# Optimization experiments

Hardware: AMD Instinct MI355X
Metric: run time of the kernel (lower is better)

Reference implementation:

```python
import jax, jax.numpy as jnp
import numpy as np

N_NODES = 100000
N_EDGES = 1600000
D = 128
HID = 256  # min(2*D, 256)
D_OUT = 128
BN_EPS = 1e-5


def setup_inputs() -> dict:
    key = jax.random.key(0)
    ks = jax.random.split(key, 16)
    s = 0.05
    inp = {
        "x": jax.random.normal(ks[0], (N_NODES, D), dtype=jnp.float32),
        "edges": jax.random.randint(ks[1], (2, N_EDGES), 0, N_NODES, dtype=jnp.int32),
        # affine_before_rnn: Linear(D, D)
        "W_aff": jax.random.normal(ks[2], (D, D), dtype=jnp.float32) * s,
        "b_aff": jnp.zeros((D,), dtype=jnp.float32),
        # GRUCell(D, D)
        "W_ih": jax.random.normal(ks[3], (3 * D, D), dtype=jnp.float32) * s,
        "b_ih": jnp.zeros((3 * D,), dtype=jnp.float32),
        "W_hh": jax.random.normal(ks[4], (3 * D, D), dtype=jnp.float32) * s,
        "b_hh": jnp.zeros((3 * D,), dtype=jnp.float32),
        # merge_layer: Linear(2*D, D)
        "W_merge": jax.random.normal(ks[5], (D, 2 * D), dtype=jnp.float32) * s,
        "b_merge": jnp.zeros((D,), dtype=jnp.float32),
        # learnable self-connection weight
        "eps": jnp.asarray(1.0, dtype=jnp.float32),
        # backbone: Linear(D, HID) -> relu -> Linear(HID, D_OUT) -> relu -> BatchNorm1d
        "W1": jax.random.normal(ks[6], (HID, D), dtype=jnp.float32) * s,
        "b1": jnp.zeros((HID,), dtype=jnp.float32),
        "W2": jax.random.normal(ks[7], (D_OUT, HID), dtype=jnp.float32) * s,
        "b2": jnp.zeros((D_OUT,), dtype=jnp.float32),
        "gamma": jnp.ones((D_OUT,), dtype=jnp.float32),
        "beta": jnp.zeros((D_OUT,), dtype=jnp.float32),
    }
    return inp


def reference(x, edges, W_aff, b_aff, W_ih, b_ih, W_hh, b_hh,
              W_merge, b_merge, eps, W1, b1, W2, b2, gamma, beta):
    src, dst = edges[0], edges[1]
    n = x.shape[0]

    # ---- aggregation 1: 'sum' -> scatter-sum of neighbor features ----
    agg_sum = jax.ops.segment_sum(x[src], dst, num_segments=n)  # (N, D)

    # ---- aggregation 2: 'rnn-max' -> affine, scatter-max, GRUCell ----
    xi = x @ W_aff.T + b_aff
    agg_max = jax.ops.segment_max(xi[src], dst, num_segments=n)  # (N, D)
    agg_max = jnp.where(jnp.isfinite(agg_max), agg_max, 0.0)  # empty segments -> 0

    # GRUCell: input = aggregated neighbors, hidden = original node features
    gi = agg_max @ W_ih.T + b_ih  # (N, 3D)
    gh = x @ W_hh.T + b_hh        # (N, 3D)
    ir, iz, inn = jnp.split(gi, 3, axis=1)
    hr, hz, hn = jnp.split(gh, 3, axis=1)
    r = jax.nn.sigmoid(ir + hr)
    z = jax.nn.sigmoid(iz + hz)
    ncand = jnp.tanh(inn + r * hn)
    rnn_out = (1.0 - z) * ncand + z * x  # (N, D)

    # ---- merge ('cat') ----
    h = jnp.concatenate([agg_sum, rnn_out], axis=1) @ W_merge.T + b_merge  # (N, D)

    # ---- learnable self-connection ----
    h = h + eps * x

    # ---- backbone: dense -> relu -> dense -> relu -> batchnorm1d (train mode) ----
    h = jax.nn.relu(h @ W1.T + b1)
    h = jax.nn.relu(h @ W2.T + b2)
    mean = jnp.mean(h, axis=0)
    var = jnp.mean(jnp.square(h - mean), axis=0)  # biased batch variance
    out = gamma * (h - mean) * jax.lax.rsqrt(var + BN_EPS) + beta
    return out
```

## Files before the change

### kernel.cpp

```cpp
#include <hip/hip_runtime.h>
#include <hip/hip_bf16.h>
#include <math.h>

using bf16 = __hip_bfloat16;
typedef __attribute__((ext_vector_type(8))) short bf16x8;
typedef __attribute__((ext_vector_type(4))) float f32x4;

__device__ __forceinline__ float b2f(unsigned short u) {
  return __uint_as_float(((unsigned)u) << 16);
}
__device__ __forceinline__ unsigned short f2b(float f) {
  bf16 h = __float2bfloat16(f);
  return *reinterpret_cast<unsigned short*>(&h);
}
__device__ __forceinline__ ushort4 f2b4(float4 v) {
  return make_ushort4(f2b(v.x), f2b(v.y), f2b(v.z), f2b(v.w));
}

__global__ __launch_bounds__(256) void mgemm_k(
    const unsigned short* __restrict__ A, int lda, const float* __restrict__ W,
    const float* __restrict__ bias, unsigned short* __restrict__ Cb, int ldc,
    int N, int M, int K) {
  constexpr int LDA = 72;
  __shared__ unsigned short As[128 * LDA];
  __shared__ unsigned short Ws[128 * LDA];

  const int tid = threadIdx.x;
  const int lane = tid & 63;
  const int wave = tid >> 6;
  const int row0 = blockIdx.y * 128;
  const int m0 = blockIdx.x * 128;
  const int rowhalf = (wave & 1) * 64;
  const int colhalf = (wave >> 1) * 64;
  const int l15 = lane & 15;
  const int quad = lane >> 4;

  f32x4 acc[4][4] = {};

  for (int kc = 0; kc < K; kc += 64) {
#pragma unroll
    for (int i = 0; i < 4; i++) {
      int idx = tid + i * 256;
      int r = idx >> 3;
      int k8 = (idx & 7) * 8;
      int row = row0 + r;
      ushort4 u0 = make_ushort4(0, 0, 0, 0), u1 = u0;
      if (row < N) {
        const unsigned short* s = A + (size_t)row * lda + kc + k8;
        u0 = *(const ushort4*)s;
        u1 = *(const ushort4*)(s + 4);
      }
      *(ushort4*)&As[r * LDA + k8] = u0;
      *(ushort4*)&As[r * LDA + k8 + 4] = u1;
    }
#pragma unroll
    for (int i = 0; i < 8; i++) {
      int idx = tid + i * 256;
      int r = idx >> 4;
      int k4 = idx & 15;
      float4 v = *(const float4*)(W + (size_t)(m0 + r) * K + kc + k4 * 4);
      *(ushort4*)&Ws[r * LDA + k4 * 4] = f2b4(v);
    }
    __syncthreads();
#pragma unroll
    for (int ks = 0; ks < 2; ks++) {
      const int ko = ks * 32 + quad * 8;
      bf16x8 af[4], wf[4];
#pragma unroll
      for (int ri = 0; ri < 4; ri++)
        af[ri] = *(const bf16x8*)&As[(rowhalf + ri * 16 + l15) * LDA + ko];
#pragma unroll
      for (int ci = 0; ci < 4; ci++)
        wf[ci] = *(const bf16x8*)&Ws[(colhalf + ci * 16 + l15) * LDA + ko];
#pragma unroll
      for (int ri = 0; ri < 4; ri++)
#pragma unroll
        for (int ci = 0; ci < 4; ci++)
          acc[ri][ci] = __builtin_amdgcn_mfma_f32_16x16x32_bf16(
              af[ri], wf[ci], acc[ri][ci], 0, 0, 0);
    }
    __syncthreads();
  }
#pragma unroll
  for (int ci = 0; ci < 4; ci++) {
    const int col = m0 + colhalf + ci * 16 + l15;
    const float bv = bias[col];
#pragma unroll
    for (int ri = 0; ri < 4; ri++) {
      const int rbase = row0 + rowhalf + ri * 16 + quad * 4;
#pragma unroll
      for (int r = 0; r < 4; r++) {
        int row = rbase + r;
        if (row >= N) continue;
        Cb[(size_t)row * ldc + col] = f2b(acc[ri][ci][r] + bv);
      }
    }
  }
}

__global__ __launch_bounds__(256, 2) void grubb_k(
    const unsigned short* __restrict__ aggm,
    const unsigned short* __restrict__ xcat,
    const unsigned short* __restrict__ aggs,
    const unsigned short* __restrict__ Wbig,
    const float* __restrict__ bias_big,
    const unsigned short* __restrict__ Wmb, const float* __restrict__ bm,
    const unsigned short* __restrict__ W1b, const float* __restrict__ b1,
    const unsigned short* __restrict__ W2b, const float* __restrict__ b2,
    const float* __restrict__ epsp, float* __restrict__ out,
    float* __restrict__ pstats, int N) {
  constexpr int LDA = 264;
  constexpr int LDH = 136;
  __shared__ unsigned short As[64 * LDA];
  __shared__ unsigned short Acat[64 * LDA];
  __shared__ float sbn[128], qbn[128];
  unsigned short* Hd = As;
  unsigned short* Hp = Acat;

  const int tid = threadIdx.x;
  const int lane = tid & 63;
  const int wave = tid >> 6;
  const int l15 = lane & 15;
  const int quad = lane >> 4;
  const int row0 = blockIdx.x * 64;
  if (tid < 128) {
    sbn[tid] = 0.f;
    qbn[tid] = 0.f;
  }
  const float ep = epsp[0];

  {
    int r = tid >> 2;
    int q = tid & 3;
    int row = row0 + r;
    int k64 = q * 64;
    uint4 u[8] = {};
    uint4 v[4] = {};
    if (row < N) {
      const unsigned short* s = (k64 < 128)
                                    ? aggm + (size_t)row * 128 + k64
                                    : xcat + (size_t)row * 256 + (k64 - 128);
#pragma unroll
      for (int i = 0; i < 8; i++) u[i] = *(const uint4*)(s + i * 8);
      const unsigned short* s2 = aggs + (size_t)row * 128 + q * 32;
#pragma unroll
      for (int i = 0; i < 4; i++) v[i] = *(const uint4*)(s2 + i * 8);
    }
#pragma unroll
    for (int i = 0; i < 8; i++) *(uint4*)&As[r * LDA + k64 + i * 8] = u[i];
#pragma unroll
    for (int i = 0; i < 4; i++) *(uint4*)&Acat[r * LDA + q * 32 + i * 8] = v[i];
  }
  __syncthreads();

  {
    const unsigned short* wptr =
        Wbig + (size_t)(wave * 128 + l15) * 256 + quad * 8;
    f32x4 acc[4][8] = {};
#pragma unroll
    for (int ks = 0; ks < 8; ks++) {
      const int ko = ks * 32 + quad * 8;
      bf16x8 af[4];
#pragma unroll
      for (int ri = 0; ri < 4; ri++)
        af[ri] = *(const bf16x8*)&As[(ri * 16 + l15) * LDA + ko];
#pragma unroll
      for (int ci = 0; ci < 8; ci++) {
        const int g = ci & 3;
        if (g == 2 && ks >= 4) continue;
        if (g == 3 && ks < 4) continue;
        bf16x8 wf = *(const bf16x8*)(wptr + (size_t)ci * 16 * 256 + ks * 32);
#pragma unroll
        for (int ri = 0; ri < 4; ri++)
          acc[ri][ci] = __builtin_amdgcn_mfma_f32_16x16x32_bf16(
              af[ri], wf, acc[ri][ci], 0, 0, 0);
      }
    }
#pragma unroll
    for (int fi = 0; fi < 2; fi++) {
      const int f = wave * 32 + fi * 16 + l15;
      const float br = bias_big[f];
      const float bz = bias_big[128 + f];
      const float bi = bias_big[256 + f];
      const float bh = bias_big[384 + f];
#pragma unroll
      for (int ri = 0; ri < 4; ri++) {
#pragma unroll
        for (int r = 0; r < 4; r++) {
          int rl = ri * 16 + quad * 4 + r;
          float rg = 1.f / (1.f + __expf(-(acc[ri][4 * fi + 0][r] + br)));
          float zg = 1.f / (1.f + __expf(-(acc[ri][4 * fi + 1][r] + bz)));
          float a =
              acc[ri][4 * fi + 2][r] + bi + rg * (acc[ri][4 * fi + 3][r] + bh);
          float t = 1.f - 2.f / (__expf(2.f * fabsf(a)) + 1.f);
          float nc = copysignf(t, a);
          float xv = b2f(As[rl * LDA + 128 + f]);
          Acat[rl * LDA + 128 + f] = f2b((1.f - zg) * nc + zg * xv);
        }
      }
    }
  }
  __syncthreads();

  f32x4 accm[4][2] = {};
  {
    const unsigned short* wptr =
        Wmb + (size_t)(wave * 32 + l15) * 256 + quad * 8;
#pragma unroll
    for (int ks = 0; ks < 8; ks++) {
      const int ko = ks * 32 + quad * 8;
      bf16x8 af[4];
#pragma unroll
      for (int ri = 0; ri < 4; ri++)
        af[ri] = *(const bf16x8*)&Acat[(ri * 16 + l15) * LDA + ko];
      bf16x8 w0 = *(const bf16x8*)(wptr + ks * 32);
      bf16x8 w1 = *(const bf16x8*)(wptr + 16 * 256 + ks * 32);
#pragma unroll
      for (int ri = 0; ri < 4; ri++) {
        accm[ri][0] = __builtin_amdgcn_mfma_f32_16x16x32_bf16(af[ri], w0,
                                                              accm[ri][0], 0, 0, 0);
        accm[ri][1] = __builtin_amdgcn_mfma_f32_16x16x32_bf16(af[ri], w1,
                                                              accm[ri][1], 0, 0, 0);
      }
    }
  }
  __syncthreads();
  {
#pragma unroll
    for (int ci = 0; ci < 2; ci++) {
      int c = wave * 32 + ci * 16 + l15;
      float bv = bm[c];
#pragma unroll
      for (int ri = 0; ri < 4; ri++) {
#pragma unroll
        for (int r = 0; r < 4; r++) {
          int rl = ri * 16 + quad * 4 + r;
          float v = accm[ri][ci][r] + bv + ep * b2f(As[rl * LDA + 128 + c]);
          Hp[rl * LDH + c] = f2b(v);
        }
      }
    }
  }
  __syncthreads();

  f32x4 acc3[4][2] = {};
#pragma unroll
  for (int hh = 0; hh < 2; hh++) {
    f32x4 acc2[4][2] = {};
    {
      const unsigned short* wptr =
          W1b + (size_t)(hh * 128 + wave * 32 + l15) * 128 + quad * 8;
#pragma unroll
      for (int ks = 0; ks < 4; ks++) {
        const int ko = ks * 32 + quad * 8;
        bf16x8 af[4];
#pragma unroll
        for (int ri = 0; ri < 4; ri++)
          af[ri] = *(const bf16x8*)&Hp[(ri * 16 + l15) * LDH + ko];
        bf16x8 w0 = *(const bf16x8*)(wptr + ks * 32);
        bf16x8 w1 = *(const bf16x8*)(wptr + 16 * 128 + ks * 32);
#pragma unroll
        for (int ri = 0; ri < 4; ri++) {
          acc2[ri][0] = __builtin_amdgcn_mfma_f32_16x16x32_bf16(
              af[ri], w0, acc2[ri][0], 0, 0, 0);
          acc2[ri][1] = __builtin_amdgcn_mfma_f32_16x16x32_bf16(
              af[ri], w1, acc2[ri][1], 0, 0, 0);
        }
      }
    }
    __syncthreads();
#pragma unroll
    for (int ci = 0; ci < 2; ci++) {
      int c = wave * 32 + ci * 16 + l15;
      float bv = b1[hh * 128 + c];
#pragma unroll
      for (int ri = 0; ri < 4; ri++) {
#pragma unroll
        for (int r = 0; r < 4; r++) {
          int rl = ri * 16 + quad * 4 + r;
          Hd[rl * LDH + c] = f2b(fmaxf(acc2[ri][ci][r] + bv, 0.f));
        }
      }
    }
    __syncthreads();
    {
      const unsigned short* wptr =
          W2b + (size_t)(wave * 32 + l15) * 256 + hh * 128 + quad * 8;
#pragma unroll
      for (int ks = 0; ks < 4; ks++) {
        const int ko = ks * 32 + quad * 8;
        bf16x8 af[4];
#pragma unroll
        for (int ri = 0; ri < 4; ri++)
          af[ri] = *(const bf16x8*)&Hd[(ri * 16 + l15) * LDH + ko];
        bf16x8 w0 = *(const bf16x8*)(wptr + ks * 32);
        bf16x8 w1 = *(const bf16x8*)(wptr + 16 * 256 + ks * 32);
#pragma unroll
        for (int ri = 0; ri < 4; ri++) {
          acc3[ri][0] = __builtin_amdgcn_mfma_f32_16x16x32_bf16(
              af[ri], w0, acc3[ri][0], 0, 0, 0);
          acc3[ri][1] = __builtin_amdgcn_mfma_f32_16x16x32_bf16(
              af[ri], w1, acc3[ri][1], 0, 0, 0);
        }
      }
    }
  }
#pragma unroll
  for (int ci = 0; ci < 2; ci++) {
    int c = wave * 32 + ci * 16 + l15;
    float bv = b2[c];
    float s = 0.f, q = 0.f;
#pragma unroll
    for (int ri = 0; ri < 4; ri++) {
#pragma unroll
      for (int r = 0; r < 4; r++) {
        int rl = ri * 16 + quad * 4 + r;
        int row = row0 + rl;
        if (row >= N) continue;
        float v = fmaxf(acc3[ri][ci][r] + bv, 0.f);
        out[(size_t)row * 128 + c] = v;
        s += v;
        q += v * v;
      }
    }
    atomicAdd(&sbn[c], s);
    atomicAdd(&qbn[c], q);
  }
  __syncthreads();
  if (tid < 128) {
    float* p = pstats + (size_t)blockIdx.x * 256;
    p[tid] = sbn[tid];
    p[128 + tid] = qbn[tid];
  }
}

__global__ __launch_bounds__(256) void bnred_k(const float* __restrict__ pstats,
                                               float* __restrict__ stats,
                                               int nb) {
  int t = threadIdx.x;
  float s = 0.f;
  for (int b = blockIdx.x; b < nb; b += gridDim.x)
    s += pstats[(size_t)b * 256 + t];
  atomicAdd(&stats[t], s);
}

__global__ __launch_bounds__(256) void prep_k(
    const float* __restrict__ W_ih, const float* __restrict__ b_ih,
    const float* __restrict__ W_hh, const float* __restrict__ b_hh,
    const float* __restrict__ Wm, const float* __restrict__ W1,
    const float* __restrict__ W2, unsigned short* __restrict__ Wbig,
    unsigned short* __restrict__ Wmb, unsigned short* __restrict__ W1b,
    unsigned short* __restrict__ W2b, float* __restrict__ bias_big,
    float* __restrict__ stats, int* __restrict__ deg, int N) {
  int idx = blockIdx.x * 256 + threadIdx.x;
  if (idx < N) deg[idx] = 0;
  if (idx < 32768) {
    int mp = idx >> 6;
    int k4 = (idx & 63) * 4;
    int w = mp >> 7, ci = (mp >> 4) & 7, l15 = mp & 15;
    int g = ci & 3, fi = ci >> 2;
    int f = w * 32 + fi * 16 + l15;
    const float* src = nullptr;
    int koff = 0;
    if (g <= 1) {
      int m = g * 128 + f;
      if (k4 < 128) { src = W_ih + (size_t)m * 128; koff = k4; }
      else          { src = W_hh + (size_t)m * 128; koff = k4 - 128; }
    } else if (g == 2) {
      if (k4 < 128) { src = W_ih + (size_t)(256 + f) * 128; koff = k4; }
    } else {
      if (k4 >= 128) { src = W_hh + (size_t)(256 + f) * 128; koff = k4 - 128; }
    }
    ushort4 o = make_ushort4(0, 0, 0, 0);
    if (src) o = f2b4(*(const float4*)(src + koff));
    *(ushort4*)&Wbig[(size_t)mp * 256 + k4] = o;
  }
  if (idx < 8192) {
    int m = idx >> 6;
    int k4 = (idx & 63) * 4;
    *(ushort4*)&Wmb[(size_t)m * 256 + k4] =
        f2b4(*(const float4*)(Wm + (size_t)m * 256 + k4));
    *(ushort4*)&W2b[(size_t)m * 256 + k4] =
        f2b4(*(const float4*)(W2 + (size_t)m * 256 + k4));
    int m2 = idx >> 5;
    int k42 = (idx & 31) * 4;
    *(ushort4*)&W1b[(size_t)m2 * 128 + k42] =
        f2b4(*(const float4*)(W1 + (size_t)m2 * 128 + k42));
  }
  if (blockIdx.x == 0) {
    int t = threadIdx.x;
    stats[t] = 0.f;
#pragma unroll
    for (int h = 0; h < 2; h++) {
      int mm = t + h * 256;
      float b;
      if (mm < 256) b = b_ih[mm] + b_hh[mm];
      else if (mm < 384) b = b_ih[mm];
      else b = b_hh[mm - 128];
      bias_big[mm] = b;
    }
  }
}

__global__ __launch_bounds__(256) void cvthist_k(
    const int* __restrict__ edges, int* __restrict__ deg, int E,
    const float* __restrict__ x, unsigned short* __restrict__ xcat,
    int ngroups, int eblk) {
  if ((int)blockIdx.x < eblk) {
    int e = blockIdx.x * 256 + threadIdx.x;
    if (e < E) atomicAdd(&deg[edges[(size_t)E + e]], 1);
  } else {
    int g = (blockIdx.x - eblk) * 256 + threadIdx.x;
    if (g >= ngroups) return;
    int n = g >> 5;
    int j = (g & 31) * 4;
    float4 v = *(const float4*)&x[(size_t)n * 128 + j];
    *(ushort4*)&xcat[(size_t)n * 256 + j] = f2b4(v);
  }
}

__global__ __launch_bounds__(256) void scan1_k(const int* __restrict__ deg,
                                               int* __restrict__ off,
                                               int* __restrict__ bsums, int N) {
  __shared__ int s[256];
  int t = threadIdx.x;
  int i = blockIdx.x * 256 + t;
  int v = (i < N) ? deg[i] : 0;
  s[t] = v;
  __syncthreads();
#pragma unroll
  for (int d = 1; d < 256; d <<= 1) {
    int u = (t >= d) ? s[t - d] : 0;
    __syncthreads();
    s[t] += u;
    __syncthreads();
  }
  if (i < N) off[i] = s[t] - v;
  if (t == 255) bsums[blockIdx.x] = s[255];
}

__global__ __launch_bounds__(512) void scan2_k(int* __restrict__ bsums,
                                               int nb) {
  __shared__ int s[512];
  int t = threadIdx.x;
  int v = (t < nb) ? bsums[t] : 0;
  s[t] = v;
  __syncthreads();
#pragma unroll
  for (int d = 1; d < 512; d <<= 1) {
    int u = (t >= d) ? s[t - d] : 0;
    __syncthreads();
    s[t] += u;
    __syncthreads();
  }
  if (t < nb) bsums[t] = s[t] - v;
}

__global__ __launch_bounds__(256) void scan3_k(int* __restrict__ off,
                                               const int* __restrict__ bsums,
                                               int* __restrict__ binoff,
                                               int* __restrict__ bincur,
                                               int N, int E, int NB) {
  int i = blockIdx.x * 256 + threadIdx.x;
  if (i < N) {
    int o = off[i] + bsums[blockIdx.x];
    off[i] = o;
    if ((i & 511) == 0) {
      binoff[i >> 9] = o;
      bincur[i >> 9] = o;
    }
  }
  if (i == 0) {
    off[N] = E;
    binoff[NB] = E;
  }
}

__global__ __launch_bounds__(256) void edgepart_k(const int* __restrict__ edges,
                                                  int* __restrict__ bincur,
                                                  int* __restrict__ part,
                                                  int E, int NB) {
  __shared__ int cnt[256];
  const int tid = threadIdx.x;
  if (tid < NB) cnt[tid] = 0;
  __syncthreads();
  int sv[16], dv[16];
  const int e0 = blockIdx.x * 4096;
#pragma unroll
  for (int i = 0; i < 16; i++) {
    int e = e0 + i * 256 + tid;
    int s = 0, d = -1;
    if (e < E) {
      s = edges[e];
      d = edges[(size_t)E + e];
    }
    sv[i] = s;
    dv[i] = d;
    if (d >= 0) atomicAdd(&cnt[d >> 9], 1);
  }
  __syncthreads();
  if (tid < NB) {
    int c = cnt[tid];
    int base = c ? atomicAdd(&bincur[tid], c) : 0;
    cnt[tid] = base;
  }
  __syncthreads();
#pragma unroll
  for (int i = 0; i < 16; i++) {
    int d = dv[i];
    if (d < 0) continue;
    int p = atomicAdd(&cnt[d >> 9], 1);
    part[p] = (sv[i] << 9) | (d & 511);
  }
}

__global__ __launch_bounds__(1024) void fill2_k(const int* __restrict__ off,
                                                const int* __restrict__ binoff,
                                                const int* __restrict__ part,
                                                int* __restrict__ bucket,
                                                int N) {
  __shared__ int scur[512];
  const int b = blockIdx.x;
  const int n0 = b << 9;
  const int tid = threadIdx.x;
  if (tid < 512) {
    int node = n0 + tid;
    scur[tid] = (node < N) ? off[node] : 0;
  }
  __syncthreads();
  const int j0 = binoff[b];
  const int j1 = binoff[b + 1];
  for (int j = j0 + tid; j < j1; j += 1024) {
    int p = part[j];
    int pos = atomicAdd(&scur[p & 511], 1);
    bucket[pos] = p >> 9;
  }
}

__global__ __launch_bounds__(256) void gather_k(
    const int* __restrict__ off, const int* __restrict__ bucket,
    const unsigned short* __restrict__ xcat, unsigned short* __restrict__ aggm,
    unsigned short* __restrict__ aggs, int N) {
  int node = blockIdx.x * 4 + (threadIdx.x >> 6);
  if (node >= N) return;
  const int lane = threadIdx.x & 63;
  const int half = lane >> 5;
  const int f = (lane & 31) * 4;
  const int j0 = off[node], jend = off[node + 1];
  float s0 = 0.f, s1 = 0.f, s2 = 0.f, s3 = 0.f;
  float m0 = -INFINITY, m1 = -INFINITY, m2 = -INFINITY, m3 = -INFINITY;
  int jj = j0 + half;
  int p0 = (jj < jend) ? bucket[jj] : 0;
  int p1 = (jj + 2 < jend) ? bucket[jj + 2] : 0;
  for (; jj < jend; jj += 2) {
    int src = p0;
    p0 = p1;
    p1 = (jj + 4 < jend) ? bucket[jj + 4] : 0;
    ushort4 a = *(const ushort4*)(xcat + (size_t)src * 256 + f);
    ushort4 b = *(const ushort4*)(xcat + (size_t)src * 256 + 128 + f);
    s0 += b2f(a.x);
    s1 += b2f(a.y);
    s2 += b2f(a.z);
    s3 += b2f(a.w);
    m0 = fmaxf(m0, b2f(b.x));
    m1 = fmaxf(m1, b2f(b.y));
    m2 = fmaxf(m2, b2f(b.z));
    m3 = fmaxf(m3, b2f(b.w));
  }
  s0 += __shfl_xor(s0, 32);
  s1 += __shfl_xor(s1, 32);
  s2 += __shfl_xor(s2, 32);
  s3 += __shfl_xor(s3, 32);
  m0 = fmaxf(m0, __shfl_xor(m0, 32));
  m1 = fmaxf(m1, __shfl_xor(m1, 32));
  m2 = fmaxf(m2, __shfl_xor(m2, 32));
  m3 = fmaxf(m3, __shfl_xor(m3, 32));
  if (half == 0) {
    bool nz = jend > j0;
    ushort4 mv = nz ? make_ushort4(f2b(m0), f2b(m1), f2b(m2), f2b(m3))
                    : make_ushort4(0, 0, 0, 0);
    *(ushort4*)&aggm[(size_t)node * 128 + f] = mv;
    *(ushort4*)&aggs[(size_t)node * 128 + f] =
        make_ushort4(f2b(s0), f2b(s1), f2b(s2), f2b(s3));
  }
}

__global__ __launch_bounds__(256) void bn_apply_k(
    float* __restrict__ out, const float* __restrict__ stats,
    const float* __restrict__ gamma, const float* __restrict__ beta,
    float invn, int nd4) {
  int g = blockIdx.x * 256 + threadIdx.x;
  if (g >= nd4) return;
  int d = (g & 31) * 4;
  float4 v = ((float4*)out)[g];
  float o[4] = {v.x, v.y, v.z, v.w};
#pragma unroll
  for (int i = 0; i < 4; i++) {
    float mean = stats[d + i] * invn;
    float var = fmaxf(stats[128 + d + i] * invn - mean * mean, 0.f);
    float sc = gamma[d + i] * rsqrtf(var + 1e-5f);
    o[i] = (o[i] - mean) * sc + beta[d + i];
  }
  ((float4*)out)[g] = make_float4(o[0], o[1], o[2], o[3]);
}

extern "C" void kernel_launch(void* const* d_in, const int* in_sizes, int n_in,
                              void* d_out, int out_size, void* d_ws,
                              size_t ws_size, hipStream_t stream) {
  (void)n_in;
  (void)out_size;
  (void)ws_size;
  const float* x = (const float*)d_in[0];
  const int* edges = (const int*)d_in[1];
  const float* W_aff = (const float*)d_in[2];
  const float* b_aff = (const float*)d_in[3];
  const float* W_ih = (const float*)d_in[4];
  const float* b_ih = (const float*)d_in[5];
  const float* W_hh = (const float*)d_in[6];
  const float* b_hh = (const float*)d_in[7];
  const float* W_merge = (const float*)d_in[8];
  const float* b_merge = (const float*)d_in[9];
  const float* epsp = (const float*)d_in[10];
  const float* W1 = (const float*)d_in[11];
  const float* b1 = (const float*)d_in[12];
  const float* W2 = (const float*)d_in[13];
  const float* b2 = (const float*)d_in[14];
  const float* gamma = (const float*)d_in[15];
  const float* beta = (const float*)d_in[16];

  const int N = in_sizes[0] / 128;
  const int E = in_sizes[1] / 2;
  const size_t nd = (size_t)N * 128;
  const int NB = (N + 511) >> 9;
  const int gblk = (N + 63) / 64;

  char* base = (char*)d_ws;
  unsigned short* xcat = (unsigned short*)base;
  unsigned short* aggs = (unsigned short*)(base + (size_t)N * 512);
  unsigned short* aggm = (unsigned short*)(base + (size_t)N * 1024);
  unsigned short* Wbig = (unsigned short*)(base + (size_t)N * 1280);
  unsigned short* Wmb = Wbig + 512 * 256;
  unsigned short* W1b = Wmb + 128 * 256;
  unsigned short* W2b = W1b + 256 * 128;
  float* bias_big = (float*)(W2b + 128 * 256);
  float* stats = bias_big + 512;
  int* deg = (int*)(stats + 512);
  int* off = deg + N;
  int* binoff = off + N + 1;
  int* bincur = binoff + NB + 1;
  int* bucket = bincur + NB;
  int* bsums = bucket + E;
  float* pstats = (float*)(bsums + ((N + 255) / 256));
  float* out = (float*)d_out;
  int* part = (int*)d_out;

  const int ny = (N + 127) / 128;
  const int nblk = (N + 255) / 256;
  const int eblk = (E + 255) / 256;
  const int cvtblk = (int)((nd / 4 + 255) / 256);
  const int pgrid = nblk > 128 ? nblk : 128;
  dim3 blk(256);

  prep_k<<<pgrid, blk, 0, stream>>>(W_ih, b_ih, W_hh, b_hh, W_merge, W1, W2,
                                    Wbig, Wmb, W1b, W2b, bias_big, stats, deg,
                                    N);
  cvthist_k<<<eblk + cvtblk, blk, 0, stream>>>(edges, deg, E, x, xcat,
                                               (int)(nd / 4), eblk);
  scan1_k<<<nblk, blk, 0, stream>>>(deg, off, bsums, N);
  scan2_k<<<1, 512, 0, stream>>>(bsums, nblk);
  scan3_k<<<nblk, blk, 0, stream>>>(off, bsums, binoff, bincur, N, E, NB);
  edgepart_k<<<(E + 4095) / 4096, blk, 0, stream>>>(edges, bincur, part, E, NB);
  fill2_k<<<NB, dim3(1024), 0, stream>>>(off, binoff, part, bucket, N);

  mgemm_k<<<dim3(1, ny), blk, 0, stream>>>(xcat, 256, W_aff, b_aff, xcat + 128,
                                           256, N, 128, 128);
  gather_k<<<(N + 3) / 4, blk, 0, stream>>>(off, bucket, xcat, aggm, aggs, N);
  grubb_k<<<gblk, blk, 0, stream>>>(aggm, xcat, aggs, Wbig, bias_big,
                                    Wmb, b_merge, W1b, b1, W2b, b2,
                                    epsp, out, pstats, N);
  bnred_k<<<64, blk, 0, stream>>>(pstats, stats, gblk);
  bn_apply_k<<<(int)((nd / 4 + 255) / 256), blk, 0, stream>>>(
      out, stats, gamma, beta, 1.f / (float)N, (int)(nd / 4));
}
```

Baseline: 563.3 us.

## Enlarge fused GRU/MLP block to 128 rows with 8 waves

The fused GRU+merge+backbone kernel now processes 128 rows per block using 512 threads (8 waves), each wave owning 16 output columns across all 128 rows instead of 32 columns across 64 rows. The goal is to reuse each weight fragment loaded from global memory across twice as many rows, cutting weight traffic per row. In exchange, LDS per block doubles, occupancy drops to one block per CU, and the grid is halved, which may reduce latency hiding.

```diff
diff --git a/kernel.cpp b/kernel.cpp
--- a/kernel.cpp
+++ b/kernel.cpp
@@ -98,7 +98,7 @@
   }
 }
 
-__global__ __launch_bounds__(256, 2) void grubb_k(
+__global__ __launch_bounds__(512, 1) void grubb_k(
     const unsigned short* __restrict__ aggm,
     const unsigned short* __restrict__ xcat,
     const unsigned short* __restrict__ aggs,
@@ -111,8 +111,8 @@
     float* __restrict__ pstats, int N) {
   constexpr int LDA = 264;
   constexpr int LDH = 136;
-  __shared__ unsigned short As[64 * LDA];
-  __shared__ unsigned short Acat[64 * LDA];
+  __shared__ unsigned short As[128 * LDA];
+  __shared__ unsigned short Acat[128 * LDA];
   __shared__ float sbn[128], qbn[128];
   unsigned short* Hd = As;
   unsigned short* Hp = Acat;
@@ -122,12 +122,13 @@
   const int wave = tid >> 6;
   const int l15 = lane & 15;
   const int quad = lane >> 4;
-  const int row0 = blockIdx.x * 64;
+  const int row0 = blockIdx.x * 128;
   if (tid < 128) {
     sbn[tid] = 0.f;
     qbn[tid] = 0.f;
   }
   const float ep = epsp[0];
+  const int f = wave * 16 + l15;
 
   {
     int r = tid >> 2;
@@ -154,177 +155,149 @@
   __syncthreads();
 
   {
-    const unsigned short* wptr =
-        Wbig + (size_t)(wave * 128 + l15) * 256 + quad * 8;
-    f32x4 acc[4][8] = {};
+    const unsigned short* wp[4];
+#pragma unroll
+    for (int g = 0; g < 4; g++)
+      wp[g] = Wbig +
+              (size_t)((wave >> 1) * 128 + (g + 4 * (wave & 1)) * 16 + l15) *
+                  256 +
+              quad * 8;
+    f32x4 acc[8][4] = {};
 #pragma unroll
     for (int ks = 0; ks < 8; ks++) {
       const int ko = ks * 32 + quad * 8;
-      bf16x8 af[4];
-#pragma unroll
-      for (int ri = 0; ri < 4; ri++)
+      bf16x8 af[8];
+#pragma unroll
+      for (int ri = 0; ri < 8; ri++)
         af[ri] = *(const bf16x8*)&As[(ri * 16 + l15) * LDA + ko];
 #pragma unroll
-      for (int ci = 0; ci < 8; ci++) {
-        const int g = ci & 3;
+      for (int g = 0; g < 4; g++) {
         if (g == 2 && ks >= 4) continue;
         if (g == 3 && ks < 4) continue;
-        bf16x8 wf = *(const bf16x8*)(wptr + (size_t)ci * 16 * 256 + ks * 32);
-#pragma unroll
-        for (int ri = 0; ri < 4; ri++)
-          acc[ri][ci] = __builtin_amdgcn_mfma_f32_16x16x32_bf16(
-              af[ri], wf, acc[ri][ci], 0, 0, 0);
-      }
-    }
-#pragma unroll
-    for (int fi = 0; fi < 2; fi++) {
-      const int f = wave * 32 + fi * 16 + l15;
-      const float br = bias_big[f];
-      const float bz = bias_big[128 + f];
-      const float bi = bias_big[256 + f];
-      const float bh = bias_big[384 + f];
-#pragma unroll
-      for (int ri = 0; ri < 4; ri++) {
+        bf16x8 wf = *(const bf16x8*)(wp[g] + ks * 32);
+#pragma unroll
+        for (int ri = 0; ri < 8; ri++)
+          acc[ri][g] = __builtin_amdgcn_mfma_f32_16x16x32_bf16(
+              af[ri], wf, acc[ri][g], 0, 0, 0);
+      }
+    }
+    const float br = bias_big[f];
+    const float bz = bias_big[128 + f];
+    const float bi = bias_big[256 + f];
+    const float bh = bias_big[384 + f];
+#pragma unroll
+    for (int ri = 0; ri < 8; ri++) {
+#pragma unroll
+      for (int r = 0; r < 4; r++) {
+        int rl = ri * 16 + quad * 4 + r;
+        float rg = 1.f / (1.f + __expf(-(acc[ri][0][r] + br)));
+        float zg = 1.f / (1.f + __expf(-(acc[ri][1][r] + bz)));
+        float a = acc[ri][2][r] + bi + rg * (acc[ri][3][r] + bh);
+        float t = 1.f - 2.f / (__expf(2.f * fabsf(a)) + 1.f);
+        float nc = copysignf(t, a);
+        float xv = b2f(As[rl * LDA + 128 + f]);
+        Acat[rl * LDA + 128 + f] = f2b((1.f - zg) * nc + zg * xv);
+      }
+    }
+  }
+  __syncthreads();
+
+  f32x4 accm[8] = {};
+  {
+    const unsigned short* wptr = Wmb + (size_t)f * 256 + quad * 8;
+#pragma unroll
+    for (int ks = 0; ks < 8; ks++) {
+      const int ko = ks * 32 + quad * 8;
+      bf16x8 w0 = *(const bf16x8*)(wptr + ks * 32);
+#pragma unroll
+      for (int ri = 0; ri < 8; ri++) {
+        bf16x8 af = *(const bf16x8*)&Acat[(ri * 16 + l15) * LDA + ko];
+        accm[ri] = __builtin_amdgcn_mfma_f32_16x16x32_bf16(af, w0, accm[ri],
+                                                           0, 0, 0);
+      }
+    }
+  }
+  __syncthreads();
+  {
+    float bv = bm[f];
+#pragma unroll
+    for (int ri = 0; ri < 8; ri++) {
+#pragma unroll
+      for (int r = 0; r < 4; r++) {
+        int rl = ri * 16 + quad * 4 + r;
+        float v = accm[ri][r] + bv + ep * b2f(As[rl * LDA + 128 + f]);
+        Hp[rl * LDH + f] = f2b(v);
+      }
+    }
+  }
+  __syncthreads();
+
+  f32x4 acc3[8] = {};
+#pragma unroll
+  for (int hh = 0; hh < 2; hh++) {
+    f32x4 acc2[8] = {};
+    {
+      const unsigned short* wptr =
+          W1b + (size_t)(hh * 128 + f) * 128 + quad * 8;
+#pragma unroll
+      for (int ks = 0; ks < 4; ks++) {
+        const int ko = ks * 32 + quad * 8;
+        bf16x8 w0 = *(const bf16x8*)(wptr + ks * 32);
+#pragma unroll
+        for (int ri = 0; ri < 8; ri++) {
+          bf16x8 af = *(const bf16x8*)&Hp[(ri * 16 + l15) * LDH + ko];
+          acc2[ri] = __builtin_amdgcn_mfma_f32_16x16x32_bf16(af, w0, acc2[ri],
+                                                             0, 0, 0);
+        }
+      }
+    }
+    __syncthreads();
+    {
+      float bv = b1[hh * 128 + f];
+#pragma unroll
+      for (int ri = 0; ri < 8; ri++) {
 #pragma unroll
         for (int r = 0; r < 4; r++) {
           int rl = ri * 16 + quad * 4 + r;
-          float rg = 1.f / (1.f + __expf(-(acc[ri][4 * fi + 0][r] + br)));
-          float zg = 1.f / (1.f + __expf(-(acc[ri][4 * fi + 1][r] + bz)));
-          float a =
-              acc[ri][4 * fi + 2][r] + bi + rg * (acc[ri][4 * fi + 3][r] + bh);
-          float t = 1.f - 2.f / (__expf(2.f * fabsf(a)) + 1.f);
-          float nc = copysignf(t, a);
-          float xv = b2f(As[rl * LDA + 128 + f]);
-          Acat[rl * LDA + 128 + f] = f2b((1.f - zg) * nc + zg * xv);
+          Hd[rl * LDH + f] = f2b(fmaxf(acc2[ri][r] + bv, 0.f));
         }
       }
     }
-  }
-  __syncthreads();
-
-  f32x4 accm[4][2] = {};
-  {
-    const unsigned short* wptr =
-        Wmb + (size_t)(wave * 32 + l15) * 256 + quad * 8;
-#pragma unroll
-    for (int ks = 0; ks < 8; ks++) {
-      const int ko = ks * 32 + quad * 8;
-      bf16x8 af[4];
-#pragma unroll
-      for (int ri = 0; ri < 4; ri++)
-        af[ri] = *(const bf16x8*)&Acat[(ri * 16 + l15) * LDA + ko];
-      bf16x8 w0 = *(const bf16x8*)(wptr + ks * 32);
-      bf16x8 w1 = *(const bf16x8*)(wptr + 16 * 256 + ks * 32);
-#pragma unroll
-      for (int ri = 0; ri < 4; ri++) {
-        accm[ri][0] = __builtin_amdgcn_mfma_f32_16x16x32_bf16(af[ri], w0,
-                                                              accm[ri][0], 0, 0, 0);
-        accm[ri][1] = __builtin_amdgcn_mfma_f32_16x16x32_bf16(af[ri], w1,
-                                                              accm[ri][1], 0, 0, 0);
-      }
-    }
-  }
-  __syncthreads();
-  {
-#pragma unroll
-    for (int ci = 0; ci < 2; ci++) {
-      int c = wave * 32 + ci * 16 + l15;
-      float bv = bm[c];
-#pragma unroll
-      for (int ri = 0; ri < 4; ri++) {
-#pragma unroll
-        for (int r = 0; r < 4; r++) {
-          int rl = ri * 16 + quad * 4 + r;
-          float v = accm[ri][ci][r] + bv + ep * b2f(As[rl * LDA + 128 + c]);
-          Hp[rl * LDH + c] = f2b(v);
-        }
-      }
-    }
-  }
-  __syncthreads();
-
-  f32x4 acc3[4][2] = {};
-#pragma unroll
-  for (int hh = 0; hh < 2; hh++) {
-    f32x4 acc2[4][2] = {};
+    __syncthreads();
     {
       const unsigned short* wptr =
-          W1b + (size_t)(hh * 128 + wave * 32 + l15) * 128 + quad * 8;
+          W2b + (size_t)f * 256 + hh * 128 + quad * 8;
 #pragma unroll
       for (int ks = 0; ks < 4; ks++) {
         const int ko = ks * 32 + quad * 8;
-        bf16x8 af[4];
-#pragma unroll
-        for (int ri = 0; ri < 4; ri++)
-          af[ri] = *(const bf16x8*)&Hp[(ri * 16 + l15) * LDH + ko];
         bf16x8 w0 = *(const bf16x8*)(wptr + ks * 32);
-        bf16x8 w1 = *(const bf16x8*)(wptr + 16 * 128 + ks * 32);
-#pragma unroll
-        for (int ri = 0; ri < 4; ri++) {
-          acc2[ri][0] = __builtin_amdgcn_mfma_f32_16x16x32_bf16(
-              af[ri], w0, acc2[ri][0], 0, 0, 0);
-          acc2[ri][1] = __builtin_amdgcn_mfma_f32_16x16x32_bf16(
-              af[ri], w1, acc2[ri][1], 0, 0, 0);
+#pragma unroll
+        for (int ri = 0; ri < 8; ri++) {
+          bf16x8 af = *(const bf16x8*)&Hd[(ri * 16 + l15) * LDH + ko];
+          acc3[ri] = __builtin_amdgcn_mfma_f32_16x16x32_bf16(af, w0, acc3[ri],
+                                                             0, 0, 0);
         }
       }
     }
-    __syncthreads();
-#pragma unroll
-    for (int ci = 0; ci < 2; ci++) {
-      int c = wave * 32 + ci * 16 + l15;
-      float bv = b1[hh * 128 + c];
-#pragma unroll
-      for (int ri = 0; ri < 4; ri++) {
-#pragma unroll
-        for (int r = 0; r < 4; r++) {
-          int rl = ri * 16 + quad * 4 + r;
-          Hd[rl * LDH + c] = f2b(fmaxf(acc2[ri][ci][r] + bv, 0.f));
-        }
-      }
-    }
-    __syncthreads();
-    {
-      const unsigned short* wptr =
-          W2b + (size_t)(wave * 32 + l15) * 256 + hh * 128 + quad * 8;
-#pragma unroll
-      for (int ks = 0; ks < 4; ks++) {
-        const int ko = ks * 32 + quad * 8;
-        bf16x8 af[4];
-#pragma unroll
-        for (int ri = 0; ri < 4; ri++)
-          af[ri] = *(const bf16x8*)&Hd[(ri * 16 + l15) * LDH + ko];
-        bf16x8 w0 = *(const bf16x8*)(wptr + ks * 32);
-        bf16x8 w1 = *(const bf16x8*)(wptr + 16 * 256 + ks * 32);
-#pragma unroll
-        for (int ri = 0; ri < 4; ri++) {
-          acc3[ri][0] = __builtin_amdgcn_mfma_f32_16x16x32_bf16(
-              af[ri], w0, acc3[ri][0], 0, 0, 0);
-          acc3[ri][1] = __builtin_amdgcn_mfma_f32_16x16x32_bf16(
-              af[ri], w1, acc3[ri][1], 0, 0, 0);
-        }
-      }
-    }
-  }
-#pragma unroll
-  for (int ci = 0; ci < 2; ci++) {
-    int c = wave * 32 + ci * 16 + l15;
-    float bv = b2[c];
+  }
+  {
+    float bv = b2[f];
     float s = 0.f, q = 0.f;
 #pragma unroll
-    for (int ri = 0; ri < 4; ri++) {
+    for (int ri = 0; ri < 8; ri++) {
 #pragma unroll
       for (int r = 0; r < 4; r++) {
         int rl = ri * 16 + quad * 4 + r;
         int row = row0 + rl;
         if (row >= N) continue;
-        float v = fmaxf(acc3[ri][ci][r] + bv, 0.f);
-        out[(size_t)row * 128 + c] = v;
+        float v = fmaxf(acc3[ri][r] + bv, 0.f);
+        out[(size_t)row * 128 + f] = v;
         s += v;
         q += v * v;
       }
     }
-    atomicAdd(&sbn[c], s);
-    atomicAdd(&qbn[c], q);
+    atomicAdd(&sbn[f], s);
+    atomicAdd(&qbn[f], q);
   }
   __syncthreads();
   if (tid < 128) {
@@ -632,7 +605,7 @@
   const int E = in_sizes[1] / 2;
   const size_t nd = (size_t)N * 128;
   const int NB = (N + 511) >> 9;
-  const int gblk = (N + 63) / 64;
+  const int gblk = (N + 127) / 128;
 
   char* base = (char*)d_ws;
   unsigned short* xcat = (unsigned short*)base;
@@ -675,9 +648,9 @@
   mgemm_k<<<dim3(1, ny), blk, 0, stream>>>(xcat, 256, W_aff, b_aff, xcat + 128,
                                            256, N, 128, 128);
   gather_k<<<(N + 3) / 4, blk, 0, stream>>>(off, bucket, xcat, aggm, aggs, N);
-  grubb_k<<<gblk, blk, 0, stream>>>(aggm, xcat, aggs, Wbig, bias_big,
-                                    Wmb, b_merge, W1b, b1, W2b, b2,
-                                    epsp, out, pstats, N);
+  grubb_k<<<gblk, dim3(512), 0, stream>>>(aggm, xcat, aggs, Wbig, bias_big,
+                                          Wmb, b_merge, W1b, b1, W2b, b2,
+                                          epsp, out, pstats, N);
   bnred_k<<<64, blk, 0, stream>>>(pstats, stats, gblk);
   bn_apply_k<<<(int)((nd / 4 + 255) / 256), blk, 0, stream>>>(
       out, stats, gamma, beta, 1.f / (float)N, (int)(nd / 4));
```

Result: slower. 579.4 us (+2.9%).
